# Kernel optimization log

Measured on AMD Instinct MI355X. Metric: run time of the kernel, lower is better.

## Reference

```python
import jax, jax.numpy as jnp
import numpy as np

CUT_DIST = 4.0            # cut_dist_bohr
FEATURES = 20
EPSILON = 1e-11
BOHR = 0.5291772105638411  # distance_mul (ase.units.Bohr)
POS_SCALE = 2.5


def setup_inputs() -> dict:
    key = jax.random.key(0)
    k1, k2 = jax.random.split(key)
    source = jax.random.normal(k1, (1, 4096, 3), dtype=jnp.float32) * POS_SCALE
    target = jax.random.normal(k2, (1, 2048, 3), dtype=jnp.float32) * POS_SCALE
    return {"source": source, "target": target}


def reference(source, target):
    # Pairwise diff between every source (probe) and target (atom): [B, N, M, 3]
    diff = target[:, None, :, :] - source[:, :, None, :]
    dist = jnp.sqrt(jnp.sum(diff * diff, axis=-1))            # [B, N, M]
    mask = dist < CUT_DIST                                    # [B, N, M] bool (self_send=True keeps d==0)
    direction = diff / (dist[..., None] + EPSILON)            # [B, N, M, 3]
    # sinc radial basis expansion on distances converted with distance_mul (Bohr)
    d = dist * BOHR + EPSILON                                 # [B, N, M]
    n = jnp.arange(1, FEATURES + 1, dtype=d.dtype)            # [F]
    d_exp = d[..., None]                                      # [B, N, M, 1]
    expansion = jnp.sin(n * jnp.pi * d_exp / CUT_DIST) / d_exp  # [B, N, M, F]
    return dist, direction, mask, expansion
```

## Files before the change

### kernel.cpp

```cpp
#include <hip/hip_runtime.h>
#include <math.h>

typedef float v4f __attribute__((ext_vector_type(4)));

#define CUT  4.0f
#define EPS  1e-11f
#define BOHR 0.5291772105638411f
#define PI_F 3.14159265358979323846f

__device__ __forceinline__ float bperm(unsigned int lane, float v) {
    return __int_as_float(
        __builtin_amdgcn_ds_bpermute((int)(lane << 2), __float_as_int(v)));
}

__global__ __launch_bounds__(256) void deepdft_expansion_kernel(
    const float* __restrict__ src,
    const float* __restrict__ tgt,
    float* __restrict__ out,
    unsigned int N, unsigned int M)
{
    const unsigned int total = N * M;

    float* __restrict__ dist_o = out;
    float* __restrict__ dir_o  = out + (size_t)total;
    float* __restrict__ mask_o = out + (size_t)4 * total;
    float* __restrict__ exp_o  = out + (size_t)5 * total;

    const unsigned int lane   = threadIdx.x & 63u;
    const unsigned int waves  = (gridDim.x * blockDim.x) >> 6;
    const unsigned int wtiles = (total + 63u) >> 6;
    const unsigned int wid    = (blockIdx.x * blockDim.x + threadIdx.x) >> 6;

    const unsigned int chunk = (wtiles + waves - 1u) / waves;
    const unsigned int tbeg  = wid * chunk;
    const unsigned int tend  = (tbeg + chunk < wtiles) ? (tbeg + chunk) : wtiles;

    for (unsigned int w = tbeg; w < tend; ++w) {
        const unsigned int base = w << 6;
        const unsigned int idx  = base + lane;
        const unsigned int cidx = (idx < total) ? idx : (total - 1u);

        unsigned int n = cidx / M;
        unsigned int m = cidx - n * M;

        float sx = src[3u*n + 0], sy = src[3u*n + 1], sz = src[3u*n + 2];
        float tx = tgt[3u*m + 0], ty = tgt[3u*m + 1], tz = tgt[3u*m + 2];

        float dx = tx - sx, dy = ty - sy, dz = tz - sz;
        float d2   = fmaf(dx, dx, fmaf(dy, dy, dz * dz));
        float dist = sqrtf(d2);
        float inv  = 1.0f / (dist + EPS);

        if (idx < total) {
            dist_o[idx] = dist;
            mask_o[idx] = (dist < CUT) ? 1.0f : 0.0f;
        }

        float ux = dx * inv, uy = dy * inv, uz = dz * inv;
        float d    = fmaf(dist, BOHR, EPS);
        float invd = 1.0f / d;
        float x    = (PI_F / CUT) * d;

        {
            float* gdir = dir_o + (size_t)3 * base;
            #pragma unroll
            for (int k = 0; k < 3; ++k) {
                unsigned int e = lane + 64u * (unsigned)k;
                unsigned int p = (e * 10923u) >> 15;
                unsigned int c = e - 3u * p;
                float vx = bperm(p, ux);
                float vy = bperm(p, uy);
                float vz = bperm(p, uz);
                float val = (c == 0u) ? vx : ((c == 1u) ? vy : vz);
                if (base + p < total) gdir[e] = val;
            }
        }

        {
            v4f* gexp = reinterpret_cast<v4f*>(exp_o) + (size_t)5 * base;
            #pragma unroll
            for (int k = 0; k < 5; ++k) {
                unsigned int j = lane + 64u * (unsigned)k;
                unsigned int p = (j * 6554u) >> 15;
                unsigned int g = j - 5u * p;
                float xv = bperm(p, x);
                float iv = bperm(p, invd);
                float n0 = (float)(4u * g + 1u);
                v4f v;
                v.x = __sinf( n0         * xv) * iv;
                v.y = __sinf((n0 + 1.0f) * xv) * iv;
                v.z = __sinf((n0 + 2.0f) * xv) * iv;
                v.w = __sinf((n0 + 3.0f) * xv) * iv;
                if (base + p < total) gexp[j] = v;
            }
        }
    }
}

extern "C" void kernel_launch(void* const* d_in, const int* in_sizes, int n_in,
                              void* d_out, int out_size, void* d_ws, size_t ws_size,
                              hipStream_t stream) {
    const float* src = (const float*)d_in[0];
    const float* tgt = (const float*)d_in[1];
    float* out = (float*)d_out;

    unsigned int N = (unsigned int)(in_sizes[0] / 3);
    unsigned int M = (unsigned int)(in_sizes[1] / 3);
    unsigned int total = N * M;

    const unsigned int block = 256;
    unsigned int wtiles = (total + 63u) >> 6;
    unsigned int blocks = (wtiles + (block / 64) - 1) / (block / 64);
    if (blocks > 2048u) blocks = 2048u;

    deepdft_expansion_kernel<<<blocks, block, 0, stream>>>(src, tgt, out, N, M);
}
```

Before: 163.7 us.

## Stage source and target coordinates in LDS and use grid-stride wave loop

Each block first copies all source and target coordinates (3*(N+M) floats, 72 KB) into shared memory. The per-element coordinate gathers then read LDS instead of global memory. The wave scheduling also changes from contiguous per-wave chunks to a grid-stride loop, and a global-memory fallback kernel is kept for inputs too large for LDS. The exchange is that every one of up to 2048 blocks reloads 72 KB, and the large LDS footprint caps blocks per CU and so limits occupancy for a store-bound kernel.

```diff
diff --git a/kernel.cpp b/kernel.cpp
--- a/kernel.cpp
+++ b/kernel.cpp
@@ -8,34 +8,57 @@
 #define BOHR 0.5291772105638411f
 #define PI_F 3.14159265358979323846f
 
+#define LDS_FLOATS 18432
+
 __device__ __forceinline__ float bperm(unsigned int lane, float v) {
     return __int_as_float(
         __builtin_amdgcn_ds_bpermute((int)(lane << 2), __float_as_int(v)));
 }
 
-__global__ __launch_bounds__(256) void deepdft_expansion_kernel(
+__global__ __launch_bounds__(256) void deepdft_staged_kernel(
     const float* __restrict__ src,
     const float* __restrict__ tgt,
     float* __restrict__ out,
     unsigned int N, unsigned int M)
 {
+    __shared__ __align__(16) float lds[LDS_FLOATS];
+    float* lsrc = lds;
+    float* ltgt = lds + 3u * N;
+
     const unsigned int total = N * M;
+    const unsigned int tid   = threadIdx.x;
+
+    {
+        const unsigned int ns = 3u * N;
+        if ((ns & 3u) == 0u) {
+            const unsigned int ns4 = ns >> 2;
+            for (unsigned int i = tid; i < ns4; i += blockDim.x)
+                ((v4f*)lsrc)[i] = ((const v4f*)src)[i];
+        } else {
+            for (unsigned int i = tid; i < ns; i += blockDim.x) lsrc[i] = src[i];
+        }
+        const unsigned int nt = 3u * M;
+        if ((ns & 3u) == 0u && (nt & 3u) == 0u) {
+            const unsigned int nt4 = nt >> 2;
+            for (unsigned int i = tid; i < nt4; i += blockDim.x)
+                ((v4f*)ltgt)[i] = ((const v4f*)tgt)[i];
+        } else {
+            for (unsigned int i = tid; i < nt; i += blockDim.x) ltgt[i] = tgt[i];
+        }
+    }
+    __syncthreads();
 
     float* __restrict__ dist_o = out;
     float* __restrict__ dir_o  = out + (size_t)total;
     float* __restrict__ mask_o = out + (size_t)4 * total;
     float* __restrict__ exp_o  = out + (size_t)5 * total;
 
-    const unsigned int lane   = threadIdx.x & 63u;
+    const unsigned int lane   = tid & 63u;
     const unsigned int waves  = (gridDim.x * blockDim.x) >> 6;
     const unsigned int wtiles = (total + 63u) >> 6;
-    const unsigned int wid    = (blockIdx.x * blockDim.x + threadIdx.x) >> 6;
-
-    const unsigned int chunk = (wtiles + waves - 1u) / waves;
-    const unsigned int tbeg  = wid * chunk;
-    const unsigned int tend  = (tbeg + chunk < wtiles) ? (tbeg + chunk) : wtiles;
-
-    for (unsigned int w = tbeg; w < tend; ++w) {
+
+    for (unsigned int w = (blockIdx.x * blockDim.x + tid) >> 6;
+         w < wtiles; w += waves) {
         const unsigned int base = w << 6;
         const unsigned int idx  = base + lane;
         const unsigned int cidx = (idx < total) ? idx : (total - 1u);
@@ -43,8 +66,8 @@
         unsigned int n = cidx / M;
         unsigned int m = cidx - n * M;
 
-        float sx = src[3u*n + 0], sy = src[3u*n + 1], sz = src[3u*n + 2];
-        float tx = tgt[3u*m + 0], ty = tgt[3u*m + 1], tz = tgt[3u*m + 2];
+        float sx = lsrc[3u*n + 0], sy = lsrc[3u*n + 1], sz = lsrc[3u*n + 2];
+        float tx = ltgt[3u*m + 0], ty = ltgt[3u*m + 1], tz = ltgt[3u*m + 2];
 
         float dx = tx - sx, dy = ty - sy, dz = tz - sz;
         float d2   = fmaf(dx, dx, fmaf(dy, dy, dz * dz));
@@ -97,6 +120,80 @@
     }
 }
 
+__global__ __launch_bounds__(256) void deepdft_global_kernel(
+    const float* __restrict__ src,
+    const float* __restrict__ tgt,
+    float* __restrict__ out,
+    unsigned int N, unsigned int M)
+{
+    const unsigned int total = N * M;
+    float* __restrict__ dist_o = out;
+    float* __restrict__ dir_o  = out + (size_t)total;
+    float* __restrict__ mask_o = out + (size_t)4 * total;
+    float* __restrict__ exp_o  = out + (size_t)5 * total;
+
+    const unsigned int lane   = threadIdx.x & 63u;
+    const unsigned int waves  = (gridDim.x * blockDim.x) >> 6;
+    const unsigned int wtiles = (total + 63u) >> 6;
+
+    for (unsigned int w = (blockIdx.x * blockDim.x + threadIdx.x) >> 6;
+         w < wtiles; w += waves) {
+        const unsigned int base = w << 6;
+        const unsigned int idx  = base + lane;
+        const unsigned int cidx = (idx < total) ? idx : (total - 1u);
+        unsigned int n = cidx / M;
+        unsigned int m = cidx - n * M;
+
+        float sx = src[3u*n + 0], sy = src[3u*n + 1], sz = src[3u*n + 2];
+        float tx = tgt[3u*m + 0], ty = tgt[3u*m + 1], tz = tgt[3u*m + 2];
+        float dx = tx - sx, dy = ty - sy, dz = tz - sz;
+        float dist = sqrtf(fmaf(dx, dx, fmaf(dy, dy, dz * dz)));
+        float inv  = 1.0f / (dist + EPS);
+
+        if (idx < total) {
+            dist_o[idx] = dist;
+            mask_o[idx] = (dist < CUT) ? 1.0f : 0.0f;
+        }
+        float ux = dx * inv, uy = dy * inv, uz = dz * inv;
+        float d    = fmaf(dist, BOHR, EPS);
+        float invd = 1.0f / d;
+        float x    = (PI_F / CUT) * d;
+
+        {
+            float* gdir = dir_o + (size_t)3 * base;
+            #pragma unroll
+            for (int k = 0; k < 3; ++k) {
+                unsigned int e = lane + 64u * (unsigned)k;
+                unsigned int p = (e * 10923u) >> 15;
+                unsigned int c = e - 3u * p;
+                float vx = bperm(p, ux);
+                float vy = bperm(p, uy);
+                float vz = bperm(p, uz);
+                float val = (c == 0u) ? vx : ((c == 1u) ? vy : vz);
+                if (base + p < total) gdir[e] = val;
+            }
+        }
+        {
+            v4f* gexp = reinterpret_cast<v4f*>(exp_o) + (size_t)5 * base;
+            #pragma unroll
+            for (int k = 0; k < 5; ++k) {
+                unsigned int j = lane + 64u * (unsigned)k;
+                unsigned int p = (j * 6554u) >> 15;
+                unsigned int g = j - 5u * p;
+                float xv = bperm(p, x);
+                float iv = bperm(p, invd);
+                float n0 = (float)(4u * g + 1u);
+                v4f v;
+                v.x = __sinf( n0         * xv) * iv;
+                v.y = __sinf((n0 + 1.0f) * xv) * iv;
+                v.z = __sinf((n0 + 2.0f) * xv) * iv;
+                v.w = __sinf((n0 + 3.0f) * xv) * iv;
+                if (base + p < total) gexp[j] = v;
+            }
+        }
+    }
+}
+
 extern "C" void kernel_launch(void* const* d_in, const int* in_sizes, int n_in,
                               void* d_out, int out_size, void* d_ws, size_t ws_size,
                               hipStream_t stream) {
@@ -113,5 +210,9 @@
     unsigned int blocks = (wtiles + (block / 64) - 1) / (block / 64);
     if (blocks > 2048u) blocks = 2048u;
 
-    deepdft_expansion_kernel<<<blocks, block, 0, stream>>>(src, tgt, out, N, M);
-}
+    if (3u * (N + M) <= (unsigned)LDS_FLOATS) {
+        deepdft_staged_kernel<<<blocks, block, 0, stream>>>(src, tgt, out, N, M);
+    } else {
+        deepdft_global_kernel<<<blocks, block, 0, stream>>>(src, tgt, out, N, M);
+    }
+}
```

After: 160.1 us. 2.2% less time.

## Split fused kernel into separate expansion and geometry kernels with grid-stride loops

Applied to the files above, without the earlier changes.

Splits the single fused kernel into two launches: one writes the sinc expansion (20 floats per pair), the other writes distance, direction and mask. Each wave now walks tiles in grid-stride order instead of a contiguous chunk. The intent is to give each kernel a simpler write stream and less register pressure, at the cost of an extra launch and recomputing the pairwise distances twice.

```diff
diff --git a/kernel.cpp b/kernel.cpp
--- a/kernel.cpp
+++ b/kernel.cpp
@@ -13,29 +13,21 @@
         __builtin_amdgcn_ds_bpermute((int)(lane << 2), __float_as_int(v)));
 }
 
-__global__ __launch_bounds__(256) void deepdft_expansion_kernel(
+__global__ __launch_bounds__(256) void deepdft_exp_kernel(
     const float* __restrict__ src,
     const float* __restrict__ tgt,
     float* __restrict__ out,
     unsigned int N, unsigned int M)
 {
     const unsigned int total = N * M;
-
-    float* __restrict__ dist_o = out;
-    float* __restrict__ dir_o  = out + (size_t)total;
-    float* __restrict__ mask_o = out + (size_t)4 * total;
-    float* __restrict__ exp_o  = out + (size_t)5 * total;
+    float* __restrict__ exp_o = out + (size_t)5 * total;
 
     const unsigned int lane   = threadIdx.x & 63u;
     const unsigned int waves  = (gridDim.x * blockDim.x) >> 6;
     const unsigned int wtiles = (total + 63u) >> 6;
-    const unsigned int wid    = (blockIdx.x * blockDim.x + threadIdx.x) >> 6;
 
-    const unsigned int chunk = (wtiles + waves - 1u) / waves;
-    const unsigned int tbeg  = wid * chunk;
-    const unsigned int tend  = (tbeg + chunk < wtiles) ? (tbeg + chunk) : wtiles;
-
-    for (unsigned int w = tbeg; w < tend; ++w) {
+    for (unsigned int w = (blockIdx.x * blockDim.x + threadIdx.x) >> 6;
+         w < wtiles; w += waves) {
         const unsigned int base = w << 6;
         const unsigned int idx  = base + lane;
         const unsigned int cidx = (idx < total) ? idx : (total - 1u);
@@ -47,8 +39,59 @@
         float tx = tgt[3u*m + 0], ty = tgt[3u*m + 1], tz = tgt[3u*m + 2];
 
         float dx = tx - sx, dy = ty - sy, dz = tz - sz;
-        float d2   = fmaf(dx, dx, fmaf(dy, dy, dz * dz));
-        float dist = sqrtf(d2);
+        float dist = sqrtf(fmaf(dx, dx, fmaf(dy, dy, dz * dz)));
+        float d    = fmaf(dist, BOHR, EPS);
+        float invd = 1.0f / d;
+        float x    = (PI_F / CUT) * d;
+
+        v4f* gexp = reinterpret_cast<v4f*>(exp_o) + (size_t)5 * base;
+        #pragma unroll
+        for (int k = 0; k < 5; ++k) {
+            unsigned int j = lane + 64u * (unsigned)k;
+            unsigned int p = (j * 6554u) >> 15;
+            unsigned int g = j - 5u * p;
+            float xv = bperm(p, x);
+            float iv = bperm(p, invd);
+            float n0 = (float)(4u * g + 1u);
+            v4f v;
+            v.x = __sinf( n0         * xv) * iv;
+            v.y = __sinf((n0 + 1.0f) * xv) * iv;
+            v.z = __sinf((n0 + 2.0f) * xv) * iv;
+            v.w = __sinf((n0 + 3.0f) * xv) * iv;
+            if (base + p < total) gexp[j] = v;
+        }
+    }
+}
+
+__global__ __launch_bounds__(256) void deepdft_geo_kernel(
+    const float* __restrict__ src,
+    const float* __restrict__ tgt,
+    float* __restrict__ out,
+    unsigned int N, unsigned int M)
+{
+    const unsigned int total = N * M;
+    float* __restrict__ dist_o = out;
+    float* __restrict__ dir_o  = out + (size_t)total;
+    float* __restrict__ mask_o = out + (size_t)4 * total;
+
+    const unsigned int lane   = threadIdx.x & 63u;
+    const unsigned int waves  = (gridDim.x * blockDim.x) >> 6;
+    const unsigned int wtiles = (total + 63u) >> 6;
+
+    for (unsigned int w = (blockIdx.x * blockDim.x + threadIdx.x) >> 6;
+         w < wtiles; w += waves) {
+        const unsigned int base = w << 6;
+        const unsigned int idx  = base + lane;
+        const unsigned int cidx = (idx < total) ? idx : (total - 1u);
+
+        unsigned int n = cidx / M;
+        unsigned int m = cidx - n * M;
+
+        float sx = src[3u*n + 0], sy = src[3u*n + 1], sz = src[3u*n + 2];
+        float tx = tgt[3u*m + 0], ty = tgt[3u*m + 1], tz = tgt[3u*m + 2];
+
+        float dx = tx - sx, dy = ty - sy, dz = tz - sz;
+        float dist = sqrtf(fmaf(dx, dx, fmaf(dy, dy, dz * dz)));
         float inv  = 1.0f / (dist + EPS);
 
         if (idx < total) {
@@ -57,42 +100,18 @@
         }
 
         float ux = dx * inv, uy = dy * inv, uz = dz * inv;
-        float d    = fmaf(dist, BOHR, EPS);
-        float invd = 1.0f / d;
-        float x    = (PI_F / CUT) * d;
 
-        {
-            float* gdir = dir_o + (size_t)3 * base;
-            #pragma unroll
-            for (int k = 0; k < 3; ++k) {
-                unsigned int e = lane + 64u * (unsigned)k;
-                unsigned int p = (e * 10923u) >> 15;
-                unsigned int c = e - 3u * p;
-                float vx = bperm(p, ux);
-                float vy = bperm(p, uy);
-                float vz = bperm(p, uz);
-                float val = (c == 0u) ? vx : ((c == 1u) ? vy : vz);
-                if (base + p < total) gdir[e] = val;
-            }
-        }
-
-        {
-            v4f* gexp = reinterpret_cast<v4f*>(exp_o) + (size_t)5 * base;
-            #pragma unroll
-            for (int k = 0; k < 5; ++k) {
-                unsigned int j = lane + 64u * (unsigned)k;
-                unsigned int p = (j * 6554u) >> 15;
-                unsigned int g = j - 5u * p;
-                float xv = bperm(p, x);
-                float iv = bperm(p, invd);
-                float n0 = (float)(4u * g + 1u);
-                v4f v;
-                v.x = __sinf( n0         * xv) * iv;
-                v.y = __sinf((n0 + 1.0f) * xv) * iv;
-                v.z = __sinf((n0 + 2.0f) * xv) * iv;
-                v.w = __sinf((n0 + 3.0f) * xv) * iv;
-                if (base + p < total) gexp[j] = v;
-            }
+        float* gdir = dir_o + (size_t)3 * base;
+        #pragma unroll
+        for (int k = 0; k < 3; ++k) {
+            unsigned int e = lane + 64u * (unsigned)k;
+            unsigned int p = (e * 10923u) >> 15;
+            unsigned int c = e - 3u * p;
+            float vx = bperm(p, ux);
+            float vy = bperm(p, uy);
+            float vz = bperm(p, uz);
+            float val = (c == 0u) ? vx : ((c == 1u) ? vy : vz);
+            if (base + p < total) gdir[e] = val;
         }
     }
 }
@@ -113,5 +132,6 @@
     unsigned int blocks = (wtiles + (block / 64) - 1) / (block / 64);
     if (blocks > 2048u) blocks = 2048u;
 
-    deepdft_expansion_kernel<<<blocks, block, 0, stream>>>(src, tgt, out, N, M);
+    deepdft_exp_kernel<<<blocks, block, 0, stream>>>(src, tgt, out, N, M);
+    deepdft_geo_kernel<<<blocks, block, 0, stream>>>(src, tgt, out, N, M);
 }
```

New measurement: 166.3 us. No clear change (+1.6%).
